# Optimization experiments

Measured on AMD Instinct MI355X. Metric: run time of the kernel, lower is better.

The kernel has to match this reference:

```python
import jax, jax.numpy as jnp
import numpy as np

N_NODES = 10000
N_EDGES = 80000
F_NODE = 16
F_EDGE = 8
BN_EPS = 1e-5


def _nnconv(x, src, dst, edge_attr, w1, b1, w2, b2, w_root, bias, cin, cout):
    # edge MLP -> per-edge weight matrices [E, cin, cout]
    h = jax.nn.relu(edge_attr @ w1 + b1) @ w2 + b2
    w = h.reshape(-1, cin, cout)
    # gather source node features, per-edge matmul
    msg = jnp.einsum('ei,eio->eo', x[src], w)  # [E, cout]
    # scatter-mean into target nodes
    deg = jax.ops.segment_sum(jnp.ones(msg.shape[0], x.dtype), dst, num_segments=N_NODES)
    agg = jax.ops.segment_sum(msg, dst, num_segments=N_NODES) / jnp.clip(deg, 1.0)[:, None]
    return x @ w_root + agg + bias


def _batchnorm(x, gamma, beta):
    m = jnp.mean(x, axis=0)
    v = jnp.mean((x - m) ** 2, axis=0)  # biased var, as torch BN training mode
    return (x - m) * jax.lax.rsqrt(v + BN_EPS) * gamma + beta


def setup_inputs() -> dict:
    key = jax.random.key(0)
    ks = jax.random.split(key, 24)
    s = 0.05
    inp = {
        'x': jax.random.normal(ks[0], (N_NODES, F_NODE), jnp.float32),
        'edge_index': jax.random.randint(ks[1], (2, N_EDGES), 0, N_NODES, jnp.int32),
        'edge_attr': jax.random.normal(ks[2], (N_EDGES, F_EDGE), jnp.float32),
        # conv1 edge MLP: F_EDGE -> 25 -> 32*F_NODE
        'nn1_w1': jax.random.normal(ks[3], (F_EDGE, 25), jnp.float32) * s,
        'nn1_b1': jnp.zeros((25,), jnp.float32),
        'nn1_w2': jax.random.normal(ks[4], (25, 32 * F_NODE), jnp.float32) * s,
        'nn1_b2': jnp.zeros((32 * F_NODE,), jnp.float32),
        'conv1_root': jax.random.normal(ks[5], (F_NODE, 32), jnp.float32) * s,
        'conv1_bias': jnp.zeros((32,), jnp.float32),
        'bn1_gamma': jnp.ones((32,), jnp.float32),
        'bn1_beta': jnp.zeros((32,), jnp.float32),
        # conv2 edge MLP: F_EDGE -> 25 -> 32*64
        'nn2_w1': jax.random.normal(ks[6], (F_EDGE, 25), jnp.float32) * s,
        'nn2_b1': jnp.zeros((25,), jnp.float32),
        'nn2_w2': jax.random.normal(ks[7], (25, 32 * 64), jnp.float32) * s,
        'nn2_b2': jnp.zeros((32 * 64,), jnp.float32),
        'conv2_root': jax.random.normal(ks[8], (32, 64), jnp.float32) * s,
        'conv2_bias': jnp.zeros((64,), jnp.float32),
        'bn2_gamma': jnp.ones((64,), jnp.float32),
        'bn2_beta': jnp.zeros((64,), jnp.float32),
        'fc1_w': jax.random.normal(ks[9], (64, 128), jnp.float32) * s,
        'fc1_b': jnp.zeros((128,), jnp.float32),
        'fc2_w': jax.random.normal(ks[10], (128, 1), jnp.float32) * s,
        'fc2_b': jnp.zeros((1,), jnp.float32),
    }
    return inp


def reference(x, edge_index, edge_attr,
              nn1_w1, nn1_b1, nn1_w2, nn1_b2, conv1_root, conv1_bias, bn1_gamma, bn1_beta,
              nn2_w1, nn2_b1, nn2_w2, nn2_b2, conv2_root, conv2_bias, bn2_gamma, bn2_beta,
              fc1_w, fc1_b, fc2_w, fc2_b):
    src, dst = edge_index[0], edge_index[1]
    h = jax.nn.elu(_nnconv(x, src, dst, edge_attr, nn1_w1, nn1_b1, nn1_w2, nn1_b2,
                           conv1_root, conv1_bias, F_NODE, 32))
    h = jax.nn.elu(_batchnorm(h, bn1_gamma, bn1_beta))
    h = jax.nn.elu(_nnconv(h, src, dst, edge_attr, nn2_w1, nn2_b1, nn2_w2, nn2_b2,
                           conv2_root, conv2_bias, 32, 64))
    h = jax.nn.elu(_batchnorm(h, bn2_gamma, bn2_beta))
    h = jax.nn.elu(h @ fc1_w + fc1_b)
    h = jax.nn.elu(h @ fc2_w + fc2_b)  # [N, 1]
    # single graph: sum over all nodes -> shape [1]
    return jnp.sum(h).reshape(1)
```

## Files before the change

### kernel.cpp

```cpp
#include <hip/hip_runtime.h>
#include <hip/hip_fp16.h>

#define N_NODES 10000
#define N_EDGES 80000
#define FN 16
#define FE 8
#define HID 25
#define C1 32
#define C2 64
#define HROW 32
#define SLOTS 40
#define SC_BLOCKS ((N_EDGES + 255) / 256)
#define NU_BLOCKS 512
#define FC_BLOCKS 640
#define TN 25
#define TB2 8
#define M1 ((HID + 1) * C1)
#define M2 ((HID + 1) * C2)
#define PRE1_BLOCKS (((M1 + 255) / 256) * (N_NODES / TN))
#define W2P_ELEMS ((HID * C1 + C1) * C2)
#define WPACK_BLOCKS (W2P_ELEMS / 256)

typedef _Float16 h16;
typedef _Float16 h16x2 __attribute__((ext_vector_type(2)));
typedef _Float16 h16x8 __attribute__((ext_vector_type(8)));

__device__ __forceinline__ float elu_f(float x) { return x > 0.f ? x : (expf(x) - 1.f); }

__device__ __forceinline__ float hdot16(const h16* __restrict__ row, const h16x2* Pk2) {
    const h16x8* rv8 = (const h16x8*)row;
    h16x2 a0 = {(h16)0.f, (h16)0.f};
    h16x2 a1 = a0, a2 = a0, a3 = a0;
#pragma unroll
    for (int q = 0; q < 4; q++) {
        h16x8 r = rv8[q];
        a0 += __builtin_shufflevector(r, r, 0, 1) * Pk2[q * 4 + 0];
        a1 += __builtin_shufflevector(r, r, 2, 3) * Pk2[q * 4 + 1];
        a2 += __builtin_shufflevector(r, r, 4, 5) * Pk2[q * 4 + 2];
        a3 += __builtin_shufflevector(r, r, 6, 7) * Pk2[q * 4 + 3];
    }
    h16x2 s = (a0 + a1) + (a2 + a3);
    return (float)s.x + (float)s.y;
}

__device__ __forceinline__ void msg1_edges(const h16x2* Pk2, int beg, int end,
                                           const int* __restrict__ ebuf,
                                           const h16* __restrict__ h1r,
                                           float* __restrict__ agg, int lane, int o) {
    int idx = beg;
    for (; idx + 7 < end; idx += 8) {
        int p[8];
#pragma unroll
        for (int j = 0; j < 8; j++) p[j] = ebuf[idx + j];
        float s[8];
#pragma unroll
        for (int j = 0; j < 8; j++) s[j] = hdot16(h1r + (size_t)(p[j] >> 14) * HROW, Pk2);
#pragma unroll
        for (int j = 0; j < 8; j += 2) {
            float va = (lane < 32) ? s[j] : s[j + 1];
            int da = (lane < 32) ? (p[j] & 0x3FFF) : (p[j + 1] & 0x3FFF);
            atomicAdd(&agg[da * C1 + o], va);
        }
    }
    for (; idx + 1 < end; idx += 2) {
        int p0 = ebuf[idx], p1 = ebuf[idx + 1];
        float s0 = hdot16(h1r + (size_t)(p0 >> 14) * HROW, Pk2);
        float s1 = hdot16(h1r + (size_t)(p1 >> 14) * HROW, Pk2);
        float va = (lane < 32) ? s0 : s1;
        int da = (lane < 32) ? (p0 & 0x3FFF) : (p1 & 0x3FFF);
        atomicAdd(&agg[da * C1 + o], va);
    }
    if (idx < end) {
        int p0 = ebuf[idx];
        float s0 = hdot16(h1r + (size_t)(p0 >> 14) * HROW, Pk2);
        if (lane < 32) atomicAdd(&agg[(p0 & 0x3FFF) * C1 + o], s0);
    }
}

__device__ __forceinline__ void msg2_edges(const h16x2* Pk2, int beg, int end,
                                           const int* __restrict__ ebuf,
                                           const h16* __restrict__ h2r,
                                           float* __restrict__ agg, int lane) {
    int idx = beg;
    for (; idx + 7 < end; idx += 8) {
        int p[8];
#pragma unroll
        for (int j = 0; j < 8; j++) p[j] = ebuf[idx + j];
        float s[8];
#pragma unroll
        for (int j = 0; j < 8; j++) s[j] = hdot16(h2r + (size_t)(p[j] >> 14) * HROW, Pk2);
#pragma unroll
        for (int j = 0; j < 8; j++) atomicAdd(&agg[(p[j] & 0x3FFF) * C2 + lane], s[j]);
    }
    for (; idx < end; idx++) {
        int p0 = ebuf[idx];
        float s0 = hdot16(h2r + (size_t)(p0 >> 14) * HROW, Pk2);
        atomicAdd(&agg[(p0 & 0x3FFF) * C2 + lane], s0);
    }
}

__device__ __forceinline__ void pre1_unit(const float* __restrict__ xin,
                                          const float* __restrict__ w2,
                                          const float* __restrict__ b2,
                                          h16* __restrict__ P, int u, int tid) {
    constexpr int MB = (M1 + 255) / 256;
    int mb = u % MB;
    int n0 = (u / MB) * TN;
    int m = mb * 256 + tid;
    if (m >= M1) return;
    int k = m >> 5, o = m & 31;
    float wreg[FN];
    if (k < HID) {
#pragma unroll
        for (int i = 0; i < FN; i++) wreg[i] = w2[(size_t)(k * FN + i) * C1 + o];
    } else {
#pragma unroll
        for (int i = 0; i < FN; i++) wreg[i] = b2[i * C1 + o];
    }
    int pmo = (k >> 1) * (2 * C1) + o * 2 + (k & 1);
    for (int n = n0; n < n0 + TN; n++) {
        const float* xr = xin + (size_t)n * FN;
        float s0 = 0.f, s1 = 0.f, s2 = 0.f, s3 = 0.f;
#pragma unroll
        for (int i = 0; i < FN; i += 4) {
            s0 += xr[i] * wreg[i];
            s1 += xr[i + 1] * wreg[i + 1];
            s2 += xr[i + 2] * wreg[i + 2];
            s3 += xr[i + 3] * wreg[i + 3];
        }
        P[(size_t)n * M1 + pmo] = (h16)((s0 + s1) + (s2 + s3));
    }
}

__global__ void k_scatter_pre1(const float* __restrict__ ea, const int* __restrict__ ei,
                               const float* __restrict__ w1a, const float* __restrict__ b1a,
                               const float* __restrict__ w1b, const float* __restrict__ b1b,
                               const float* __restrict__ x, const float* __restrict__ w2a,
                               const float* __restrict__ b2a, const float* __restrict__ w2b,
                               const float* __restrict__ b2b,
                               int* __restrict__ cnt_src, int* __restrict__ cnt_dst,
                               int* __restrict__ ebuf, h16* __restrict__ h1r,
                               h16* __restrict__ h2r, h16* __restrict__ P1,
                               h16* __restrict__ w2p) {
    int tid = threadIdx.x;
    int bid = blockIdx.x;
    if (bid >= SC_BLOCKS + PRE1_BLOCKS) {
        int idx = (bid - SC_BLOCKS - PRE1_BLOCKS) * 256 + tid;
        w2p[idx] = (h16)(idx < HID * C1 * C2 ? w2b[idx] : b2b[idx - HID * C1 * C2]);
        return;
    }
    if (bid >= SC_BLOCKS) {
        pre1_unit(x, w2a, b2a, P1, bid - SC_BLOCKS, tid);
        return;
    }
    __shared__ float sw1a[FE * HID], sw1b[FE * HID], sb1a[HID], sb1b[HID];
    for (int i = tid; i < FE * HID; i += 256) { sw1a[i] = w1a[i]; sw1b[i] = w1b[i]; }
    if (tid < HID) { sb1a[tid] = b1a[tid]; sb1b[tid] = b1b[tid]; }
    __syncthreads();
    int e = bid * 256 + tid;
    if (e >= N_EDGES) return;
    float a[FE];
    {
        float4 va = *(const float4*)(ea + (size_t)e * FE);
        float4 vb = *(const float4*)(ea + (size_t)e * FE + 4);
        a[0] = va.x; a[1] = va.y; a[2] = va.z; a[3] = va.w;
        a[4] = vb.x; a[5] = vb.y; a[6] = vb.z; a[7] = vb.w;
    }
    int src = ei[e], dst = ei[N_EDGES + e];
    int slot = atomicAdd(&cnt_src[src], 1);
    if (slot < SLOTS) ebuf[src * SLOTS + slot] = (e << 14) | dst;
    atomicAdd(&cnt_dst[dst], 1);
    h16 b1buf[HROW], b2buf[HROW];
#pragma unroll
    for (int k = 0; k < HID; k++) {
        float s1 = sb1a[k], s2 = sb1b[k];
#pragma unroll
        for (int i = 0; i < FE; i++) { s1 += a[i] * sw1a[i * HID + k]; s2 += a[i] * sw1b[i * HID + k]; }
        b1buf[k] = (h16)fmaxf(s1, 0.f);
        b2buf[k] = (h16)fmaxf(s2, 0.f);
    }
    b1buf[25] = (h16)1.f; b2buf[25] = (h16)1.f;
#pragma unroll
    for (int k = 26; k < HROW; k++) { b1buf[k] = (h16)0.f; b2buf[k] = (h16)0.f; }
    h16x8* h1p = (h16x8*)(h1r + (size_t)e * HROW);
    h16x8* h2p = (h16x8*)(h2r + (size_t)e * HROW);
#pragma unroll
    for (int q = 0; q < 4; q++) {
        h1p[q] = ((const h16x8*)b1buf)[q];
        h2p[q] = ((const h16x8*)b2buf)[q];
    }
}

__global__ void k_conv1(const h16x2* __restrict__ P1p, const int* __restrict__ cnt_src,
                        const int* __restrict__ ebuf, const h16* __restrict__ h1r,
                        float* __restrict__ agg) {
    int lane = threadIdx.x & 63;
    int o = lane & 31;
    int n = __builtin_amdgcn_readfirstlane(blockIdx.x * 4 + (threadIdx.x >> 6));
    if (n >= N_NODES) return;
    h16x2 Pk2[16];
    const h16x2* Pr = P1p + (size_t)n * (M1 / 2) + o;
#pragma unroll
    for (int kk = 0; kk < 13; kk++) Pk2[kk] = Pr[kk * C1];
#pragma unroll
    for (int kk = 13; kk < 16; kk++) Pk2[kk] = (h16x2){(h16)0.f, (h16)0.f};
    int deg = cnt_src[n];
    deg = deg < SLOTS ? deg : SLOTS;
    msg1_edges(Pk2, n * SLOTS, n * SLOTS + deg, ebuf, h1r, agg, lane, o);
}

template <int CIN, int COUT>
__global__ void k_node_update(const float* __restrict__ xin, const float* __restrict__ root,
                              const float* __restrict__ bias, const float* __restrict__ agg,
                              const int* __restrict__ degi, float* __restrict__ act,
                              float* __restrict__ s1g, float* __restrict__ s2g,
                              float* zero_out) {
    __shared__ float l1[256], l2[256];
    int tid = threadIdx.x;
    if (zero_out && blockIdx.x == 0 && tid == 0) *zero_out = 0.f;
    int o = tid % COUT;
    float b = bias[o];
    float rcol[CIN];
#pragma unroll
    for (int i = 0; i < CIN; i++) rcol[i] = root[i * COUT + o];
    float acc1 = 0.f, acc2 = 0.f;
    for (int t = blockIdx.x * 256 + tid; t < N_NODES * COUT; t += NU_BLOCKS * 256) {
        int n = t / COUT;
        const float* xr = xin + (size_t)n * CIN;
        float s0 = b, s1 = 0.f, s2 = 0.f, s3 = 0.f;
#pragma unroll
        for (int i = 0; i < CIN; i += 4) {
            s0 += xr[i]     * rcol[i];
            s1 += xr[i + 1] * rcol[i + 1];
            s2 += xr[i + 2] * rcol[i + 2];
            s3 += xr[i + 3] * rcol[i + 3];
        }
        float s = (s0 + s1) + (s2 + s3);
        s += agg[t] / fmaxf((float)degi[n], 1.0f);
        float a = elu_f(s);
        act[t] = a;
        acc1 += a; acc2 += a * a;
    }
    l1[tid] = acc1; l2[tid] = acc2;
    __syncthreads();
    for (int s = 128; s >= COUT; s >>= 1) {
        if (tid < s) { l1[tid] += l1[tid + s]; l2[tid] += l2[tid + s]; }
        __syncthreads();
    }
    if (tid < COUT) { atomicAdd(&s1g[tid], l1[tid]); atomicAdd(&s2g[tid], l2[tid]); }
}

__global__ __launch_bounds__(256, 5)
void k_conv2(const float* __restrict__ a1, const float* __restrict__ s1g,
             const float* __restrict__ s2g, const float* __restrict__ gamma,
             const float* __restrict__ beta, const h16* __restrict__ w2p,
             const int* __restrict__ cnt_src, const int* __restrict__ ebuf,
             const h16* __restrict__ h2r, float* __restrict__ agg,
             float* __restrict__ h1v) {
    __shared__ h16 Pl_h[TB2 * M2];
    __shared__ h16 xs_h[C1 * TB2];
    int tid = threadIdx.x;
    int n0 = blockIdx.x * TB2;
    {
        int n = tid >> 5, o = tid & 31;
        float m = s1g[o] * (1.0f / N_NODES);
        float v = s2g[o] * (1.0f / N_NODES) - m * m;
        float sc = rsqrtf(v + 1e-5f) * gamma[o];
        float sh = beta[o] - m * sc;
        float val = elu_f(a1[(size_t)n0 * C1 + tid] * sc + sh);
        xs_h[o * TB2 + n] = (h16)val;
        h1v[(size_t)n0 * C1 + tid] = val;
    }
    __syncthreads();
    const h16x8* xsv = (const h16x8*)xs_h;
#pragma unroll
    for (int mm = 0; mm < 7; mm++) {
        int m = mm * 256 + tid;
        if (m < M2) {
            int k = m >> 6, o = m & 63;
            const h16* bp = w2p + (size_t)(k * C1) * C2 + o;
            h16x2 wh[C1];
#pragma unroll
            for (int i = 0; i < C1; i++) { h16 w = bp[i * C2]; wh[i] = (h16x2){w, w}; }
            h16x2 acc0 = {(h16)0.f, (h16)0.f};
            h16x2 acc1 = acc0, acc2 = acc0, acc3 = acc0;
#pragma unroll
            for (int i = 0; i < C1; i++) {
                h16x8 xv = xsv[i];
                acc0 += __builtin_shufflevector(xv, xv, 0, 1) * wh[i];
                acc1 += __builtin_shufflevector(xv, xv, 2, 3) * wh[i];
                acc2 += __builtin_shufflevector(xv, xv, 4, 5) * wh[i];
                acc3 += __builtin_shufflevector(xv, xv, 6, 7) * wh[i];
            }
            int pmo = (k >> 1) * (2 * C2) + o * 2 + (k & 1);
            h16* Plr = Pl_h + pmo;
            Plr[0 * M2] = acc0.x; Plr[1 * M2] = acc0.y;
            Plr[2 * M2] = acc1.x; Plr[3 * M2] = acc1.y;
            Plr[4 * M2] = acc2.x; Plr[5 * M2] = acc2.y;
            Plr[6 * M2] = acc3.x; Plr[7 * M2] = acc3.y;
        }
    }
    __syncthreads();
    const h16x2* Plp = (const h16x2*)Pl_h;
    int lane = tid & 63, wv = tid >> 6;
    for (int dn = wv; dn < TB2; dn += 4) {
        int n = n0 + dn;
        h16x2 Pk2[16];
#pragma unroll
        for (int kk = 0; kk < 13; kk++) Pk2[kk] = Plp[dn * (M2 / 2) + kk * C2 + lane];
#pragma unroll
        for (int kk = 13; kk < 16; kk++) Pk2[kk] = (h16x2){(h16)0.f, (h16)0.f};
        int deg = cnt_src[n];
        deg = deg < SLOTS ? deg : SLOTS;
        msg2_edges(Pk2, n * SLOTS, n * SLOTS + deg, ebuf, h2r, agg, lane);
    }
}

__global__ void k_fc_sum(const float* __restrict__ a2,
                         const float* __restrict__ s1g, const float* __restrict__ s2g,
                         const float* __restrict__ gamma, const float* __restrict__ beta,
                         const float* __restrict__ fc1w, const float* __restrict__ fc1b,
                         const float* __restrict__ fc2w, const float* __restrict__ fc2b,
                         float* __restrict__ out) {
    int tid = threadIdx.x;
    int lane = tid & 63;
    int wave = tid >> 6;
    float m = s1g[lane] * (1.0f / N_NODES);
    float var = s2g[lane] * (1.0f / N_NODES) - m * m;
    float scale = rsqrtf(var + 1e-5f) * gamma[lane];
    float shift = beta[lane] - m * scale;
    float b0 = fc1b[lane], b1 = fc1b[lane + 64];
    float w0 = fc2w[lane], w1 = fc2w[lane + 64];
    float fb = fc2b[0];
    float acc = 0.f;
    for (int n = blockIdx.x * 4 + wave; n < N_NODES; n += FC_BLOCKS * 4) {
        float hval = elu_f(a2[(size_t)n * C2 + lane] * scale + shift);
        float s0 = b0, s1 = b1;
#pragma unroll
        for (int i = 0; i < C2; i++) {
            float hv = __shfl(hval, i);
            s0 += hv * fc1w[i * 128 + lane];
            s1 += hv * fc1w[i * 128 + 64 + lane];
        }
        float v = elu_f(s0) * w0 + elu_f(s1) * w1;
#pragma unroll
        for (int off2 = 32; off2 > 0; off2 >>= 1) v += __shfl_down(v, off2);
        if (lane == 0) acc += elu_f(v + fb);
    }
    __shared__ float lds[4];
    if (lane == 0) lds[wave] = acc;
    __syncthreads();
    if (tid == 0) atomicAdd(out, lds[0] + lds[1] + lds[2] + lds[3]);
}

extern "C" void kernel_launch(void* const* d_in, const int* in_sizes, int n_in,
                              void* d_out, int out_size, void* d_ws, size_t ws_size,
                              hipStream_t stream) {
    const float* x       = (const float*)d_in[0];
    const int*   ei      = (const int*)d_in[1];
    const float* ea      = (const float*)d_in[2];
    const float* nn1_w1  = (const float*)d_in[3];
    const float* nn1_b1  = (const float*)d_in[4];
    const float* nn1_w2  = (const float*)d_in[5];
    const float* nn1_b2  = (const float*)d_in[6];
    const float* c1_root = (const float*)d_in[7];
    const float* c1_bias = (const float*)d_in[8];
    const float* bn1_g   = (const float*)d_in[9];
    const float* bn1_b   = (const float*)d_in[10];
    const float* nn2_w1  = (const float*)d_in[11];
    const float* nn2_b1  = (const float*)d_in[12];
    const float* nn2_w2  = (const float*)d_in[13];
    const float* nn2_b2  = (const float*)d_in[14];
    const float* c2_root = (const float*)d_in[15];
    const float* c2_bias = (const float*)d_in[16];
    const float* bn2_g   = (const float*)d_in[17];
    const float* bn2_b   = (const float*)d_in[18];
    const float* fc1_w   = (const float*)d_in[19];
    const float* fc1_b   = (const float*)d_in[20];
    const float* fc2_w   = (const float*)d_in[21];
    const float* fc2_b   = (const float*)d_in[22];
    float* out = (float*)d_out;

    char* ws = (char*)d_ws;
    size_t off = 0;
    auto alloc = [&](size_t nbytes) -> void* {
        void* q = (void*)(ws + off);
        off += nbytes;
        off = (off + 255) & ~(size_t)255;
        return q;
    };
    int*   cnt_src = (int*)alloc(N_NODES * 4);
    int*   cnt_dst = (int*)alloc(N_NODES * 4);
    float* agg1    = (float*)alloc((size_t)N_NODES * C1 * 4);
    float* agg2    = (float*)alloc((size_t)N_NODES * C2 * 4);
    float* bn1_s1  = (float*)alloc(C1 * 4);
    float* bn1_s2  = (float*)alloc(C1 * 4);
    float* bn2_s1  = (float*)alloc(C2 * 4);
    float* bn2_s2  = (float*)alloc(C2 * 4);
    size_t zero_bytes = off;
    int*   ebuf = (int*)alloc((size_t)N_NODES * SLOTS * 4);
    h16*   h1r  = (h16*)alloc((size_t)N_EDGES * HROW * 2);
    h16*   h2r  = (h16*)alloc((size_t)N_EDGES * HROW * 2);
    h16*   P1   = (h16*)alloc((size_t)N_NODES * M1 * 2);
    h16*   w2p  = (h16*)alloc((size_t)W2P_ELEMS * 2);
    float* a1   = (float*)alloc((size_t)N_NODES * C1 * 4);
    float* h1v  = (float*)alloc((size_t)N_NODES * C1 * 4);
    float* a2   = (float*)alloc((size_t)N_NODES * C2 * 4);
    (void)ws_size; (void)in_sizes; (void)n_in; (void)out_size;

    hipMemsetAsync(d_ws, 0, zero_bytes, stream);

    k_scatter_pre1<<<SC_BLOCKS + PRE1_BLOCKS + WPACK_BLOCKS, 256, 0, stream>>>(
        ea, ei, nn1_w1, nn1_b1, nn2_w1, nn2_b1, x, nn1_w2, nn1_b2, nn2_w2, nn2_b2,
        cnt_src, cnt_dst, ebuf, h1r, h2r, P1, w2p);
    k_conv1<<<(N_NODES + 3) / 4, 256, 0, stream>>>((const h16x2*)P1, cnt_src, ebuf, h1r, agg1);
    k_node_update<FN, C1><<<NU_BLOCKS, 256, 0, stream>>>(x, c1_root, c1_bias, agg1,
                                                         cnt_dst, a1, bn1_s1, bn1_s2, nullptr);
    k_conv2<<<N_NODES / TB2, 256, 0, stream>>>(a1, bn1_s1, bn1_s2, bn1_g, bn1_b,
                                               w2p, cnt_src, ebuf, h2r, agg2, h1v);
    k_node_update<C1, C2><<<NU_BLOCKS, 256, 0, stream>>>(h1v, c2_root, c2_bias, agg2,
                                                         cnt_dst, a2, bn2_s1, bn2_s2, out);
    k_fc_sum<<<FC_BLOCKS, 256, 0, stream>>>(a2, bn2_s1, bn2_s2, bn2_g, bn2_b,
                                            fc1_w, fc1_b, fc2_w, fc2_b, out);
}
```

Before: 237.4 us.

## Scatter messages with packed fp16 atomics and two outputs per lane

Switches both NNConv aggregation buffers from fp32 to fp16 and scatters with global_atomic_pk_add_f16, so one atomic carries two output channels. Each lane now computes two output channels for one edge while several edges run in parallel across the wavefront. The edge loops lose their 8-way unrolled batching. The aim is to halve the atomic count and the aggregation memory traffic. The cost is precision: 16-bit accumulation of up to 40 messages per node can lose accuracy. The conv2 launch bound drops to 4 waves to make room for more registers.

```diff
diff --git a/kernel.cpp b/kernel.cpp
--- a/kernel.cpp
+++ b/kernel.cpp
@@ -23,79 +23,61 @@
 
 typedef _Float16 h16;
 typedef _Float16 h16x2 __attribute__((ext_vector_type(2)));
+typedef _Float16 h16x4 __attribute__((ext_vector_type(4)));
 typedef _Float16 h16x8 __attribute__((ext_vector_type(8)));
 
 __device__ __forceinline__ float elu_f(float x) { return x > 0.f ? x : (expf(x) - 1.f); }
 
-__device__ __forceinline__ float hdot16(const h16* __restrict__ row, const h16x2* Pk2) {
-    const h16x8* rv8 = (const h16x8*)row;
-    h16x2 a0 = {(h16)0.f, (h16)0.f};
-    h16x2 a1 = a0, a2 = a0, a3 = a0;
-#pragma unroll
-    for (int q = 0; q < 4; q++) {
-        h16x8 r = rv8[q];
-        a0 += __builtin_shufflevector(r, r, 0, 1) * Pk2[q * 4 + 0];
-        a1 += __builtin_shufflevector(r, r, 2, 3) * Pk2[q * 4 + 1];
-        a2 += __builtin_shufflevector(r, r, 4, 5) * Pk2[q * 4 + 2];
-        a3 += __builtin_shufflevector(r, r, 6, 7) * Pk2[q * 4 + 3];
-    }
-    h16x2 s = (a0 + a1) + (a2 + a3);
-    return (float)s.x + (float)s.y;
-}
-
-__device__ __forceinline__ void msg1_edges(const h16x2* Pk2, int beg, int end,
+__device__ __forceinline__ void atomic_pk_add(h16* addr, h16x2 v) {
+    uint32_t d;
+    __builtin_memcpy(&d, &v, 4);
+    asm volatile("global_atomic_pk_add_f16 %0, %1, off"
+                 :: "v"((unsigned long long)(uintptr_t)addr), "v"(d) : "memory");
+}
+
+#define ACC_PAIR(rq, jj, kk)                                            \
+    {                                                                   \
+        h16x2 rp = __builtin_shufflevector(rq, rq, 2 * jj, 2 * jj + 1); \
+        h16x4 pp = PkAB[kk];                                            \
+        accA += rp * __builtin_shufflevector(pp, pp, 0, 1);             \
+        accB += rp * __builtin_shufflevector(pp, pp, 2, 3);             \
+    }
+
+__device__ __forceinline__ h16x2 hdot2(const h16* __restrict__ row, const h16x4* PkAB) {
+    const h16x8* rv = (const h16x8*)row;
+    h16x8 r0 = rv[0], r1 = rv[1], r2 = rv[2], r3 = rv[3];
+    h16x2 accA = {(h16)0.f, (h16)0.f};
+    h16x2 accB = accA;
+    ACC_PAIR(r0, 0, 0) ACC_PAIR(r0, 1, 1) ACC_PAIR(r0, 2, 2) ACC_PAIR(r0, 3, 3)
+    ACC_PAIR(r1, 0, 4) ACC_PAIR(r1, 1, 5) ACC_PAIR(r1, 2, 6) ACC_PAIR(r1, 3, 7)
+    ACC_PAIR(r2, 0, 8) ACC_PAIR(r2, 1, 9) ACC_PAIR(r2, 2, 10) ACC_PAIR(r2, 3, 11)
+    ACC_PAIR(r3, 0, 12)
+    return (h16x2){(h16)(accA.x + accA.y), (h16)(accB.x + accB.y)};
+}
+
+__device__ __forceinline__ void msg1_edges(const h16x4* PkAB, int beg, int end,
                                            const int* __restrict__ ebuf,
                                            const h16* __restrict__ h1r,
-                                           float* __restrict__ agg, int lane, int o) {
-    int idx = beg;
-    for (; idx + 7 < end; idx += 8) {
-        int p[8];
-#pragma unroll
-        for (int j = 0; j < 8; j++) p[j] = ebuf[idx + j];
-        float s[8];
-#pragma unroll
-        for (int j = 0; j < 8; j++) s[j] = hdot16(h1r + (size_t)(p[j] >> 14) * HROW, Pk2);
-#pragma unroll
-        for (int j = 0; j < 8; j += 2) {
-            float va = (lane < 32) ? s[j] : s[j + 1];
-            int da = (lane < 32) ? (p[j] & 0x3FFF) : (p[j + 1] & 0x3FFF);
-            atomicAdd(&agg[da * C1 + o], va);
-        }
-    }
-    for (; idx + 1 < end; idx += 2) {
-        int p0 = ebuf[idx], p1 = ebuf[idx + 1];
-        float s0 = hdot16(h1r + (size_t)(p0 >> 14) * HROW, Pk2);
-        float s1 = hdot16(h1r + (size_t)(p1 >> 14) * HROW, Pk2);
-        float va = (lane < 32) ? s0 : s1;
-        int da = (lane < 32) ? (p0 & 0x3FFF) : (p1 & 0x3FFF);
-        atomicAdd(&agg[da * C1 + o], va);
-    }
-    if (idx < end) {
-        int p0 = ebuf[idx];
-        float s0 = hdot16(h1r + (size_t)(p0 >> 14) * HROW, Pk2);
-        if (lane < 32) atomicAdd(&agg[(p0 & 0x3FFF) * C1 + o], s0);
-    }
-}
-
-__device__ __forceinline__ void msg2_edges(const h16x2* Pk2, int beg, int end,
+                                           h16* __restrict__ agg, int q, int esel) {
+    for (int idx = beg; idx < end; idx += 4) {
+        int off = idx + esel;
+        bool act = off < end;
+        int pe = ebuf[act ? off : beg];
+        h16x2 out = hdot2(h1r + (size_t)(pe >> 14) * HROW, PkAB);
+        if (act) atomic_pk_add(agg + (size_t)(pe & 0x3FFF) * C1 + 2 * q, out);
+    }
+}
+
+__device__ __forceinline__ void msg2_edges(const h16x4* PkAB, int beg, int end,
                                            const int* __restrict__ ebuf,
                                            const h16* __restrict__ h2r,
-                                           float* __restrict__ agg, int lane) {
-    int idx = beg;
-    for (; idx + 7 < end; idx += 8) {
-        int p[8];
-#pragma unroll
-        for (int j = 0; j < 8; j++) p[j] = ebuf[idx + j];
-        float s[8];
-#pragma unroll
-        for (int j = 0; j < 8; j++) s[j] = hdot16(h2r + (size_t)(p[j] >> 14) * HROW, Pk2);
-#pragma unroll
-        for (int j = 0; j < 8; j++) atomicAdd(&agg[(p[j] & 0x3FFF) * C2 + lane], s[j]);
-    }
-    for (; idx < end; idx++) {
-        int p0 = ebuf[idx];
-        float s0 = hdot16(h2r + (size_t)(p0 >> 14) * HROW, Pk2);
-        atomicAdd(&agg[(p0 & 0x3FFF) * C2 + lane], s0);
+                                           h16* __restrict__ agg, int q, int esel) {
+    for (int idx = beg; idx < end; idx += 2) {
+        int off = idx + esel;
+        bool act = off < end;
+        int pe = ebuf[act ? off : beg];
+        h16x2 out = hdot2(h2r + (size_t)(pe >> 14) * HROW, PkAB);
+        if (act) atomic_pk_add(agg + (size_t)(pe & 0x3FFF) * C2 + 2 * q, out);
     }
 }
 
@@ -193,25 +175,24 @@
 
 __global__ void k_conv1(const h16x2* __restrict__ P1p, const int* __restrict__ cnt_src,
                         const int* __restrict__ ebuf, const h16* __restrict__ h1r,
-                        float* __restrict__ agg) {
+                        h16* __restrict__ agg) {
     int lane = threadIdx.x & 63;
-    int o = lane & 31;
+    int q = lane & 15;
+    int esel = lane >> 4;
     int n = __builtin_amdgcn_readfirstlane(blockIdx.x * 4 + (threadIdx.x >> 6));
     if (n >= N_NODES) return;
-    h16x2 Pk2[16];
-    const h16x2* Pr = P1p + (size_t)n * (M1 / 2) + o;
-#pragma unroll
-    for (int kk = 0; kk < 13; kk++) Pk2[kk] = Pr[kk * C1];
-#pragma unroll
-    for (int kk = 13; kk < 16; kk++) Pk2[kk] = (h16x2){(h16)0.f, (h16)0.f};
+    h16x4 PkAB[13];
+    const h16x4* Pr4 = (const h16x4*)(P1p + (size_t)n * (M1 / 2));
+#pragma unroll
+    for (int kk = 0; kk < 13; kk++) PkAB[kk] = Pr4[kk * (C1 / 2) + q];
     int deg = cnt_src[n];
     deg = deg < SLOTS ? deg : SLOTS;
-    msg1_edges(Pk2, n * SLOTS, n * SLOTS + deg, ebuf, h1r, agg, lane, o);
+    msg1_edges(PkAB, n * SLOTS, n * SLOTS + deg, ebuf, h1r, agg, q, esel);
 }
 
 template <int CIN, int COUT>
 __global__ void k_node_update(const float* __restrict__ xin, const float* __restrict__ root,
-                              const float* __restrict__ bias, const float* __restrict__ agg,
+                              const float* __restrict__ bias, const h16* __restrict__ agg,
                               const int* __restrict__ degi, float* __restrict__ act,
                               float* __restrict__ s1g, float* __restrict__ s2g,
                               float* zero_out) {
@@ -236,7 +217,7 @@
             s3 += xr[i + 3] * rcol[i + 3];
         }
         float s = (s0 + s1) + (s2 + s3);
-        s += agg[t] / fmaxf((float)degi[n], 1.0f);
+        s += (float)agg[t] / fmaxf((float)degi[n], 1.0f);
         float a = elu_f(s);
         act[t] = a;
         acc1 += a; acc2 += a * a;
@@ -250,12 +231,12 @@
     if (tid < COUT) { atomicAdd(&s1g[tid], l1[tid]); atomicAdd(&s2g[tid], l2[tid]); }
 }
 
-__global__ __launch_bounds__(256, 5)
+__global__ __launch_bounds__(256, 4)
 void k_conv2(const float* __restrict__ a1, const float* __restrict__ s1g,
              const float* __restrict__ s2g, const float* __restrict__ gamma,
              const float* __restrict__ beta, const h16* __restrict__ w2p,
              const int* __restrict__ cnt_src, const int* __restrict__ ebuf,
-             const h16* __restrict__ h2r, float* __restrict__ agg,
+             const h16* __restrict__ h2r, h16* __restrict__ agg,
              float* __restrict__ h1v) {
     __shared__ h16 Pl_h[TB2 * M2];
     __shared__ h16 xs_h[C1 * TB2];
@@ -301,18 +282,18 @@
         }
     }
     __syncthreads();
-    const h16x2* Plp = (const h16x2*)Pl_h;
+    const h16x4* Pl4 = (const h16x4*)Pl_h;
     int lane = tid & 63, wv = tid >> 6;
+    int q = lane & 31;
+    int esel = lane >> 5;
     for (int dn = wv; dn < TB2; dn += 4) {
         int n = n0 + dn;
-        h16x2 Pk2[16];
-#pragma unroll
-        for (int kk = 0; kk < 13; kk++) Pk2[kk] = Plp[dn * (M2 / 2) + kk * C2 + lane];
-#pragma unroll
-        for (int kk = 13; kk < 16; kk++) Pk2[kk] = (h16x2){(h16)0.f, (h16)0.f};
+        h16x4 PkAB[13];
+#pragma unroll
+        for (int kk = 0; kk < 13; kk++) PkAB[kk] = Pl4[dn * (M2 / 4) + kk * (C2 / 2) + q];
         int deg = cnt_src[n];
         deg = deg < SLOTS ? deg : SLOTS;
-        msg2_edges(Pk2, n * SLOTS, n * SLOTS + deg, ebuf, h2r, agg, lane);
+        msg2_edges(PkAB, n * SLOTS, n * SLOTS + deg, ebuf, h2r, agg, q, esel);
     }
 }
 
@@ -391,8 +372,8 @@
     };
     int*   cnt_src = (int*)alloc(N_NODES * 4);
     int*   cnt_dst = (int*)alloc(N_NODES * 4);
-    float* agg1    = (float*)alloc((size_t)N_NODES * C1 * 4);
-    float* agg2    = (float*)alloc((size_t)N_NODES * C2 * 4);
+    h16*   agg1    = (h16*)alloc((size_t)N_NODES * C1 * 2);
+    h16*   agg2    = (h16*)alloc((size_t)N_NODES * C2 * 2);
     float* bn1_s1  = (float*)alloc(C1 * 4);
     float* bn1_s2  = (float*)alloc(C1 * 4);
     float* bn2_s1  = (float*)alloc(C2 * 4);
```

Result: faster. 215.6 us, median of 2 (-9.2%).
